# Optimization experiments

Measured on AMD Instinct MI355X. Metric: run time of the kernel, lower is better.

Reference implementation:

```python
import jax, jax.numpy as jnp
import numpy as np

NV, NE, H, P = 50000, 10000, 256, 400000

def setup_inputs() -> dict:
    key = jax.random.key(0)
    ks = jax.random.split(key, 16)
    s = 1.0 / np.sqrt(H)
    return {
        "v": jax.random.normal(ks[0], (NV, H), jnp.float32),
        "e": jax.random.normal(ks[1], (NE, H), jnp.float32),
        "W_v2e_w": jax.random.normal(ks[2], (H, H), jnp.float32) * s,
        "W_v2e_b": jnp.zeros((H,), jnp.float32),
        "W_e2v_w": jax.random.normal(ks[3], (H, H), jnp.float32) * s,
        "W_e2v_b": jnp.zeros((H,), jnp.float32),
        "n_weight": jax.random.uniform(ks[4], (NV, 1), jnp.float32),
        "e_weight": jax.random.uniform(ks[5], (NE, 1), jnp.float32),
        "n_reg_weight": jax.random.uniform(ks[6], (P, 1), jnp.float32),
        "e_reg_weight": jax.random.uniform(ks[7], (P, 1), jnp.float32),
        "e_reg_sum": jax.random.uniform(ks[8], (NE, 1), jnp.float32) + 1.0,  # positive normalizer
        "n_reg_sum": jax.random.uniform(ks[9], (NV, 1), jnp.float32) + 1.0,
        "pairs_v": jax.random.randint(ks[10], (P,), 0, NV, jnp.int32),  # ve_lists[:,0]
        "eidx": jax.random.randint(ks[11], (P,), 0, NE, jnp.int32),
        "pairs_e": jax.random.randint(ks[12], (P,), 0, NE, jnp.int32),  # ve_lists[:,1]
        "vidx": jax.random.randint(ks[13], (P,), 0, NV, jnp.int32),
    }

def reference(v, e, W_v2e_w, W_v2e_b, W_e2v_w, W_e2v_b, n_weight, e_weight,
              n_reg_weight, e_reg_weight, e_reg_sum, n_reg_sum,
              pairs_v, eidx, pairs_e, vidx):
    # v2e: dense transform on vertices, gather per incidence, scatter-add into edges
    ve = jax.nn.relu(v @ W_v2e_w.T + W_v2e_b)            # [NV,H]
    v_acc = v * n_weight                                 # v *= n_weight * v_fac(=1)
    msg_ve = (ve * n_weight)[pairs_v] * n_reg_weight     # [P,H]
    e_out = e.at[eidx].add(msg_ve) / e_reg_sum           # [NE,H]
    # e2v: dense transform on edges, gather per incidence, scatter-add into vertices
    ev = jax.nn.relu(e_out @ W_e2v_w.T + W_e2v_b)        # [NE,H]
    msg_ev = (ev * e_weight)[pairs_e] * e_reg_weight     # [P,H]
    v_out = v_acc.at[vidx].add(msg_ev) / n_reg_sum       # [NV,H]
    return v_out, e_out
```

## Files before the change

kernel.cpp:

```cpp
#include <hip/hip_runtime.h>
#include <stdint.h>

#define NV 50000
#define NE 10000
#define HD 256
#define NP 400000

#define SE 88
#define SV 36

#define NCH 128
#define CHP (NP / NCH)
#define NW  15000
#define NWE 2500
#define NWV 12500

#define PREP_HBLK NCH
#define PREP_WBLK 16

typedef short short8 __attribute__((ext_vector_type(8)));
typedef short short4v __attribute__((ext_vector_type(4)));
typedef float f32x4 __attribute__((ext_vector_type(4)));

__device__ __forceinline__ short f2bf(float f) {
    unsigned int u = __builtin_bit_cast(unsigned int, f);
    u += 0x7FFFu + ((u >> 16) & 1u);
    return (short)(u >> 16);
}
__device__ __forceinline__ float bf2f(short s) {
    unsigned int u = ((unsigned int)(unsigned short)s) << 16;
    return __builtin_bit_cast(float, u);
}

__global__ __launch_bounds__(1024) void prep_kernel(
    const float* __restrict__ W1, const float* __restrict__ W2,
    const int* __restrict__ eidx, const int* __restrict__ vidx,
    short* __restrict__ W_bf,
    int* __restrict__ cnt8)
{
    __shared__ int h[NW];
    int b = blockIdx.x;
    int tid = threadIdx.x;
    if (b < PREP_HBLK) {
        for (int w = tid; w < NW; w += 1024) h[w] = 0;
        __syncthreads();
        int base = b * CHP;
        for (int k = tid; k < CHP; k += 1024) {
            int p = base + k;
            int er = eidx[p];
            atomicAdd((unsigned*)&h[er >> 2], 1u << ((er & 3) * 8));
            int rv = 10000 + vidx[p];
            atomicAdd((unsigned*)&h[rv >> 2], 1u << ((rv & 3) * 8));
        }
        __syncthreads();
        for (int w = tid; w < NW; w += 1024) cnt8[b * NW + w] = h[w];
    } else {
        size_t i = (size_t)(b - PREP_HBLK) * 8192 + (size_t)tid * 8;
        const float* src = (i < 65536) ? (W1 + i) : (W2 + (i - 65536));
        float4 a0 = *(const float4*)src;
        float4 a1 = *(const float4*)(src + 4);
        short8 s;
        s[0] = f2bf(a0.x); s[1] = f2bf(a0.y); s[2] = f2bf(a0.z); s[3] = f2bf(a0.w);
        s[4] = f2bf(a1.x); s[5] = f2bf(a1.y); s[6] = f2bf(a1.z); s[7] = f2bf(a1.w);
        *(short8*)(W_bf + i) = s;
    }
}

__global__ __launch_bounds__(256) void scan_kernel(
    int* __restrict__ cnt8, int* __restrict__ cnt_e, int* __restrict__ cnt_v)
{
    int w = blockIdx.x * 256 + threadIdx.x;
    if (w >= NW) return;
    unsigned acc = 0;
#pragma unroll 8
    for (int c = 0; c < NCH; ++c) {
        unsigned x = (unsigned)cnt8[c * NW + w];
        cnt8[c * NW + w] = (int)acc;
        acc += x;
    }
    int r0 = w * 4;
    int4 t;
    t.x = acc & 0xFF; t.y = (acc >> 8) & 0xFF; t.z = (acc >> 16) & 0xFF; t.w = acc >> 24;
    if (r0 < 10000) *(int4*)&cnt_e[r0] = t;
    else            *(int4*)&cnt_v[r0 - 10000] = t;
}

__global__ __launch_bounds__(1024) void place_kernel(
    const int* __restrict__ eidx, const int* __restrict__ vidx,
    const int* __restrict__ pairs_v, const int* __restrict__ n_reg_w_bits,
    const int* __restrict__ pairs_e, const int* __restrict__ e_reg_w_bits,
    const int* __restrict__ cnt8,
    int2* __restrict__ bkt_e, int2* __restrict__ bkt_v)
{
    __shared__ int h[NWV];
    int b = blockIdx.x;
    int tid = threadIdx.x;
    if (b < NCH) {
        int c = b;
        for (int w = tid; w < NWE; w += 1024) h[w] = cnt8[c * NW + w];
        __syncthreads();
        int base = c * CHP;
        for (int k = tid; k < CHP; k += 1024) {
            int p = base + k;
            int er = eidx[p];
            unsigned old = atomicAdd((unsigned*)&h[er >> 2], 1u << ((er & 3) * 8));
            int s = (old >> ((er & 3) * 8)) & 0xFF;
            if (s < SE) bkt_e[er * SE + s] = make_int2(pairs_v[p], n_reg_w_bits[p]);
        }
    } else {
        int c = b - NCH;
        for (int w = tid; w < NWV; w += 1024) h[w] = cnt8[c * NW + NWE + w];
        __syncthreads();
        int base = c * CHP;
        for (int k = tid; k < CHP; k += 1024) {
            int p = base + k;
            int vr = vidx[p];
            unsigned old = atomicAdd((unsigned*)&h[vr >> 2], 1u << ((vr & 3) * 8));
            int s = (old >> ((vr & 3) * 8)) & 0xFF;
            if (s < SV) bkt_v[vr * SV + s] = make_int2(pairs_e[p], e_reg_w_bits[p]);
        }
    }
}

__global__ __launch_bounds__(256) void gemm_rs(
    const void* __restrict__ Av, int a_bf,
    const short* __restrict__ Wb,
    const float* __restrict__ bias,
    const float* __restrict__ rowscale,
    short* __restrict__ out,
    short* __restrict__ a_out,
    int M)
{
    __shared__ short As[64 * 256];
    __shared__ short Ws[64 * 256];
    const int tid  = threadIdx.x;
    const int row0 = blockIdx.x * 64;

#pragma unroll
    for (int it = 0; it < 8; ++it) {
        int cl = it * 256 + tid;
        int r  = cl >> 5;
        int c  = cl & 31;
        int gr0 = row0 + r;
        int gr  = gr0 < M ? gr0 : M - 1;
        short8 ap;
        if (a_bf) {
            ap = *(const short8*)((const short*)Av + (size_t)gr * HD + (c << 3));
        } else {
            const float* asrc = (const float*)Av + (size_t)gr * HD + (c << 3);
            float4 a0 = *(const float4*)asrc;
            float4 a1 = *(const float4*)(asrc + 4);
            ap[0] = f2bf(a0.x); ap[1] = f2bf(a0.y); ap[2] = f2bf(a0.z); ap[3] = f2bf(a0.w);
            ap[4] = f2bf(a1.x); ap[5] = f2bf(a1.y); ap[6] = f2bf(a1.z); ap[7] = f2bf(a1.w);
            if (a_out && gr0 < M)
                *(short8*)(a_out + (size_t)gr0 * HD + (c << 3)) = ap;
        }
        *(short8*)&As[(r << 8) + ((c ^ (r & 7)) << 3)] = ap;
    }

    const int lane = tid & 63;
    const int wv   = tid >> 6;
    const int m16  = lane & 15;
    const int quad = lane >> 4;
    const int arow = (wv << 4) + m16;

    for (int ct = 0; ct < 4; ++ct) {
        __syncthreads();
#pragma unroll
        for (int it = 0; it < 8; ++it) {
            int cl = it * 256 + tid;
            int r  = cl >> 5;
            int c  = cl & 31;
            short8 wp = *(const short8*)(Wb + (size_t)((ct << 6) + r) * HD + (c << 3));
            *(short8*)&Ws[(r << 8) + ((c ^ (r & 7)) << 3)] = wp;
        }
        __syncthreads();

        f32x4 acc[4];
#pragma unroll
        for (int nt = 0; nt < 4; ++nt) acc[nt] = (f32x4){0.f, 0.f, 0.f, 0.f};

#pragma unroll
        for (int ks = 0; ks < 8; ++ks) {
            int c = (ks << 2) + quad;
            short8 afr = *(const short8*)&As[(arow << 8) + ((c ^ (arow & 7)) << 3)];
#pragma unroll
            for (int nt = 0; nt < 4; ++nt) {
                int brow = (nt << 4) + m16;
                short8 bfr = *(const short8*)&Ws[(brow << 8) + ((c ^ (m16 & 7)) << 3)];
                acc[nt] = __builtin_amdgcn_mfma_f32_16x16x32_bf16(afr, bfr, acc[nt], 0, 0, 0);
            }
        }

#pragma unroll
        for (int r = 0; r < 4; ++r) {
            int row = row0 + (wv << 4) + (quad << 2) + r;
            if (row < M) {
                float rs = rowscale[row];
#pragma unroll
                for (int nt = 0; nt < 4; ++nt) {
                    int col = (ct << 6) + (nt << 4) + m16;
                    float val = acc[nt][r] + bias[col];
                    val = fmaxf(val, 0.0f) * rs;
                    out[(size_t)row * HD + col] = f2bf(val);
                }
            }
        }
    }
}

__device__ __forceinline__ void gather_win(
    const short* __restrict__ msg, int src, int wb, int cnt, int lane,
    float4& A, float4& B)
{
    int j = 0;
    for (; j + 8 <= cnt; j += 8) {
        int s0 = __shfl(src, j),     s1 = __shfl(src, j + 1);
        int s2 = __shfl(src, j + 2), s3 = __shfl(src, j + 3);
        int s4 = __shfl(src, j + 4), s5 = __shfl(src, j + 5);
        int s6 = __shfl(src, j + 6), s7 = __shfl(src, j + 7);
        float w0 = __builtin_bit_cast(float, __shfl(wb, j));
        float w1 = __builtin_bit_cast(float, __shfl(wb, j + 1));
        float w2 = __builtin_bit_cast(float, __shfl(wb, j + 2));
        float w3 = __builtin_bit_cast(float, __shfl(wb, j + 3));
        float w4 = __builtin_bit_cast(float, __shfl(wb, j + 4));
        float w5 = __builtin_bit_cast(float, __shfl(wb, j + 5));
        float w6 = __builtin_bit_cast(float, __shfl(wb, j + 6));
        float w7 = __builtin_bit_cast(float, __shfl(wb, j + 7));
        short4v m0 = *(const short4v*)(msg + ((size_t)s0 << 8) + (lane << 2));
        short4v m1 = *(const short4v*)(msg + ((size_t)s1 << 8) + (lane << 2));
        short4v m2 = *(const short4v*)(msg + ((size_t)s2 << 8) + (lane << 2));
        short4v m3 = *(const short4v*)(msg + ((size_t)s3 << 8) + (lane << 2));
        short4v m4 = *(const short4v*)(msg + ((size_t)s4 << 8) + (lane << 2));
        short4v m5 = *(const short4v*)(msg + ((size_t)s5 << 8) + (lane << 2));
        short4v m6 = *(const short4v*)(msg + ((size_t)s6 << 8) + (lane << 2));
        short4v m7 = *(const short4v*)(msg + ((size_t)s7 << 8) + (lane << 2));
        A.x += bf2f(m0[0]) * w0; A.y += bf2f(m0[1]) * w0;
        A.z += bf2f(m0[2]) * w0; A.w += bf2f(m0[3]) * w0;
        B.x += bf2f(m1[0]) * w1; B.y += bf2f(m1[1]) * w1;
        B.z += bf2f(m1[2]) * w1; B.w += bf2f(m1[3]) * w1;
        A.x += bf2f(m2[0]) * w2; A.y += bf2f(m2[1]) * w2;
        A.z += bf2f(m2[2]) * w2; A.w += bf2f(m2[3]) * w2;
        B.x += bf2f(m3[0]) * w3; B.y += bf2f(m3[1]) * w3;
        B.z += bf2f(m3[2]) * w3; B.w += bf2f(m3[3]) * w3;
        A.x += bf2f(m4[0]) * w4; A.y += bf2f(m4[1]) * w4;
        A.z += bf2f(m4[2]) * w4; A.w += bf2f(m4[3]) * w4;
        B.x += bf2f(m5[0]) * w5; B.y += bf2f(m5[1]) * w5;
        B.z += bf2f(m5[2]) * w5; B.w += bf2f(m5[3]) * w5;
        A.x += bf2f(m6[0]) * w6; A.y += bf2f(m6[1]) * w6;
        A.z += bf2f(m6[2]) * w6; A.w += bf2f(m6[3]) * w6;
        B.x += bf2f(m7[0]) * w7; B.y += bf2f(m7[1]) * w7;
        B.z += bf2f(m7[2]) * w7; B.w += bf2f(m7[3]) * w7;
    }
    for (; j + 2 <= cnt; j += 2) {
        int s0 = __shfl(src, j), s1 = __shfl(src, j + 1);
        float w0 = __builtin_bit_cast(float, __shfl(wb, j));
        float w1 = __builtin_bit_cast(float, __shfl(wb, j + 1));
        short4v m0 = *(const short4v*)(msg + ((size_t)s0 << 8) + (lane << 2));
        short4v m1 = *(const short4v*)(msg + ((size_t)s1 << 8) + (lane << 2));
        A.x += bf2f(m0[0]) * w0; A.y += bf2f(m0[1]) * w0;
        A.z += bf2f(m0[2]) * w0; A.w += bf2f(m0[3]) * w0;
        B.x += bf2f(m1[0]) * w1; B.y += bf2f(m1[1]) * w1;
        B.z += bf2f(m1[2]) * w1; B.w += bf2f(m1[3]) * w1;
    }
    if (j < cnt) {
        int s0 = __shfl(src, j);
        float w0 = __builtin_bit_cast(float, __shfl(wb, j));
        short4v m0 = *(const short4v*)(msg + ((size_t)s0 << 8) + (lane << 2));
        A.x += bf2f(m0[0]) * w0; A.y += bf2f(m0[1]) * w0;
        A.z += bf2f(m0[2]) * w0; A.w += bf2f(m0[3]) * w0;
    }
}

__global__ __launch_bounds__(256) void gather_e(
    const short* __restrict__ msg,
    const int2* __restrict__ bkt,
    const int* __restrict__ cnt,
    const float* __restrict__ e_in, const float* __restrict__ reg_sum,
    float* __restrict__ out, short* __restrict__ out_bf)
{
    int r    = (blockIdx.x << 2) + (threadIdx.x >> 6);
    int lane = threadIdx.x & 63;
    int i0 = r * SE;
    int2 q = bkt[i0 + lane];
    int n = cnt[r]; n = n < SE ? n : SE;
    float4 A = ((const float4*)(e_in + (size_t)r * HD))[lane];
    float4 B = {0.f, 0.f, 0.f, 0.f};
    float inv = 1.0f / reg_sum[r];
    int n0 = n < 64 ? n : 64;
    gather_win(msg, q.x, q.y, n0, lane, A, B);
    if (n > 64) {
        int2 q2 = make_int2(0, 0);
        if (lane < SE - 64) q2 = bkt[i0 + 64 + lane];
        gather_win(msg, q2.x, q2.y, n - 64, lane, A, B);
    }
    float4 acc;
    acc.x = (A.x + B.x) * inv; acc.y = (A.y + B.y) * inv;
    acc.z = (A.z + B.z) * inv; acc.w = (A.w + B.w) * inv;
    ((float4*)(out + (size_t)r * HD))[lane] = acc;
    if (out_bf) {
        short4v s;
        s[0] = f2bf(acc.x); s[1] = f2bf(acc.y); s[2] = f2bf(acc.z); s[3] = f2bf(acc.w);
        *(short4v*)(out_bf + (size_t)r * HD + (lane << 2)) = s;
    }
}

__global__ __launch_bounds__(256) void gather_v(
    const short* __restrict__ msg,
    const int2* __restrict__ bkt,
    const int* __restrict__ cnt,
    const float* __restrict__ v_f32, const short* __restrict__ v_bf,
    const float* __restrict__ n_w,
    const float* __restrict__ reg_sum, float* __restrict__ out)
{
    int r    = (blockIdx.x << 2) + (threadIdx.x >> 6);
    int lane = threadIdx.x & 63;
    int i0 = r * SV;
    int2 q = bkt[i0 + lane];
    int n = cnt[r]; n = n < SV ? n : SV;
    float nw = n_w[r];
    float inv = 1.0f / reg_sum[r];
    float4 a;
    if (v_bf) {
        short4v b = *(const short4v*)(v_bf + (size_t)r * HD + (lane << 2));
        a.x = bf2f(b[0]); a.y = bf2f(b[1]); a.z = bf2f(b[2]); a.w = bf2f(b[3]);
    } else {
        a = ((const float4*)(v_f32 + (size_t)r * HD))[lane];
    }
    float4 A; A.x = a.x * nw; A.y = a.y * nw; A.z = a.z * nw; A.w = a.w * nw;
    float4 B = {0.f, 0.f, 0.f, 0.f};
    gather_win(msg, q.x, q.y, n, lane, A, B);
    float4 acc;
    acc.x = (A.x + B.x) * inv; acc.y = (A.y + B.y) * inv;
    acc.z = (A.z + B.z) * inv; acc.w = (A.w + B.w) * inv;
    ((float4*)(out + (size_t)r * HD))[lane] = acc;
}

extern "C" void kernel_launch(void* const* d_in, const int* in_sizes, int n_in,
                              void* d_out, int out_size, void* d_ws, size_t ws_size,
                              hipStream_t stream) {
    const float* v   = (const float*)d_in[0];
    const float* e   = (const float*)d_in[1];
    const float* W1  = (const float*)d_in[2];
    const float* b1  = (const float*)d_in[3];
    const float* W2  = (const float*)d_in[4];
    const float* b2  = (const float*)d_in[5];
    const float* n_weight     = (const float*)d_in[6];
    const float* e_weight     = (const float*)d_in[7];
    const float* n_reg_weight = (const float*)d_in[8];
    const float* e_reg_weight = (const float*)d_in[9];
    const float* e_reg_sum    = (const float*)d_in[10];
    const float* n_reg_sum    = (const float*)d_in[11];
    const int* pairs_v = (const int*)d_in[12];
    const int* eidx    = (const int*)d_in[13];
    const int* pairs_e = (const int*)d_in[14];
    const int* vidx    = (const int*)d_in[15];

    float* out      = (float*)d_out;
    float* v_region = out;
    float* e_region = out + (size_t)NV * HD;

    char* ws = (char*)d_ws;
    size_t o = 0;
    short* msg     = (short*)(ws + o); o += (size_t)NV * HD * 2;
    int2*  bkt_e   = (int2*)(ws + o);  o += ((size_t)NE * SE + 64) * 8;
    int2*  bkt_v   = (int2*)(ws + o);  o += ((size_t)NV * SV + 64) * 8;
    short* W_bf    = (short*)(ws + o); o += (size_t)2 * 65536 * 2;
    int*   cnt8    = (int*)(ws + o);
    short* e_bf    = (short*)(ws + o); o += (size_t)NCH * NW * 4;
    int*   cnt_e   = (int*)(ws + o);   o += (size_t)NE * 4;
    int*   cnt_v   = (int*)(ws + o);   o += (size_t)NV * 4;
    size_t o_opt = o;
    short* v_bf    = (short*)(ws + o_opt);
    size_t need_full = o_opt + (size_t)NV * HD * 2;
    const int full = (ws_size >= need_full);

    prep_kernel<<<PREP_HBLK + PREP_WBLK, 1024, 0, stream>>>(
        W1, W2, eidx, vidx, W_bf, cnt8);
    scan_kernel<<<(NW + 255) / 256, 256, 0, stream>>>(cnt8, cnt_e, cnt_v);
    place_kernel<<<2 * NCH, 1024, 0, stream>>>(
        eidx, vidx, pairs_v, (const int*)n_reg_weight,
        pairs_e, (const int*)e_reg_weight, cnt8, bkt_e, bkt_v);

    gemm_rs<<<(NV + 63) / 64, 256, 0, stream>>>(
        (const void*)v, 0, W_bf, b1, n_weight, msg, full ? v_bf : (short*)0, NV);
    gather_e<<<NE / 4, 256, 0, stream>>>(msg, bkt_e, cnt_e,
        e, e_reg_sum, e_region, e_bf);
    gemm_rs<<<(NE + 63) / 64, 256, 0, stream>>>(
        (const void*)e_bf, 1, W_bf + 65536, b2, e_weight, msg, (short*)0, NE);
    gather_v<<<NV / 4, 256, 0, stream>>>(msg, bkt_v, cnt_v,
        v, full ? v_bf : (short*)0, n_weight, n_reg_sum, v_region);
}
```

Before: 282.5 us.

## Load GEMM operands directly into registers and drop bf16 copy of v

Measured after the change: 322.7 us. 1.14x slower.

```diff
diff --git a/kernel.cpp b/kernel.cpp
--- a/kernel.cpp
+++ b/kernel.cpp
@@ -128,67 +128,49 @@
     const float* __restrict__ bias,
     const float* __restrict__ rowscale,
     short* __restrict__ out,
-    short* __restrict__ a_out,
     int M)
 {
-    __shared__ short As[64 * 256];
-    __shared__ short Ws[64 * 256];
     const int tid  = threadIdx.x;
-    const int row0 = blockIdx.x * 64;
-
-#pragma unroll
-    for (int it = 0; it < 8; ++it) {
-        int cl = it * 256 + tid;
-        int r  = cl >> 5;
-        int c  = cl & 31;
-        int gr0 = row0 + r;
-        int gr  = gr0 < M ? gr0 : M - 1;
-        short8 ap;
-        if (a_bf) {
-            ap = *(const short8*)((const short*)Av + (size_t)gr * HD + (c << 3));
-        } else {
-            const float* asrc = (const float*)Av + (size_t)gr * HD + (c << 3);
-            float4 a0 = *(const float4*)asrc;
-            float4 a1 = *(const float4*)(asrc + 4);
-            ap[0] = f2bf(a0.x); ap[1] = f2bf(a0.y); ap[2] = f2bf(a0.z); ap[3] = f2bf(a0.w);
-            ap[4] = f2bf(a1.x); ap[5] = f2bf(a1.y); ap[6] = f2bf(a1.z); ap[7] = f2bf(a1.w);
-            if (a_out && gr0 < M)
-                *(short8*)(a_out + (size_t)gr0 * HD + (c << 3)) = ap;
-        }
-        *(short8*)&As[(r << 8) + ((c ^ (r & 7)) << 3)] = ap;
-    }
-
     const int lane = tid & 63;
     const int wv   = tid >> 6;
     const int m16  = lane & 15;
     const int quad = lane >> 4;
     const int arow = (wv << 4) + m16;
+    const int row0 = blockIdx.x * 64;
+    int gr0 = row0 + arow;
+    int gr  = gr0 < M ? gr0 : M - 1;
+
+    short8 a_frag[8];
+    if (a_bf) {
+        const short* asrc = (const short*)Av + (size_t)gr * HD + (quad << 3);
+#pragma unroll
+        for (int ks = 0; ks < 8; ++ks)
+            a_frag[ks] = *(const short8*)(asrc + (ks << 5));
+    } else {
+        const float* asrc = (const float*)Av + (size_t)gr * HD + (quad << 3);
+#pragma unroll
+        for (int ks = 0; ks < 8; ++ks) {
+            float4 a0 = *(const float4*)(asrc + (ks << 5));
+            float4 a1 = *(const float4*)(asrc + (ks << 5) + 4);
+            short8 ap;
+            ap[0] = f2bf(a0.x); ap[1] = f2bf(a0.y); ap[2] = f2bf(a0.z); ap[3] = f2bf(a0.w);
+            ap[4] = f2bf(a1.x); ap[5] = f2bf(a1.y); ap[6] = f2bf(a1.z); ap[7] = f2bf(a1.w);
+            a_frag[ks] = ap;
+        }
+    }
 
     for (int ct = 0; ct < 4; ++ct) {
-        __syncthreads();
-#pragma unroll
-        for (int it = 0; it < 8; ++it) {
-            int cl = it * 256 + tid;
-            int r  = cl >> 5;
-            int c  = cl & 31;
-            short8 wp = *(const short8*)(Wb + (size_t)((ct << 6) + r) * HD + (c << 3));
-            *(short8*)&Ws[(r << 8) + ((c ^ (r & 7)) << 3)] = wp;
-        }
-        __syncthreads();
-
         f32x4 acc[4];
 #pragma unroll
         for (int nt = 0; nt < 4; ++nt) acc[nt] = (f32x4){0.f, 0.f, 0.f, 0.f};
 
+        const short* wbase = Wb + (size_t)((ct << 6) + m16) * HD + (quad << 3);
 #pragma unroll
         for (int ks = 0; ks < 8; ++ks) {
-            int c = (ks << 2) + quad;
-            short8 afr = *(const short8*)&As[(arow << 8) + ((c ^ (arow & 7)) << 3)];
 #pragma unroll
             for (int nt = 0; nt < 4; ++nt) {
-                int brow = (nt << 4) + m16;
-                short8 bfr = *(const short8*)&Ws[(brow << 8) + ((c ^ (m16 & 7)) << 3)];
-                acc[nt] = __builtin_amdgcn_mfma_f32_16x16x32_bf16(afr, bfr, acc[nt], 0, 0, 0);
+                short8 bfr = *(const short8*)(wbase + ((size_t)(nt << 4) * HD) + (ks << 5));
+                acc[nt] = __builtin_amdgcn_mfma_f32_16x16x32_bf16(a_frag[ks], bfr, acc[nt], 0, 0, 0);
             }
         }
 
@@ -309,7 +291,7 @@
     const short* __restrict__ msg,
     const int2* __restrict__ bkt,
     const int* __restrict__ cnt,
-    const float* __restrict__ v_f32, const short* __restrict__ v_bf,
+    const float* __restrict__ v_f32,
     const float* __restrict__ n_w,
     const float* __restrict__ reg_sum, float* __restrict__ out)
 {
@@ -320,13 +302,7 @@
     int n = cnt[r]; n = n < SV ? n : SV;
     float nw = n_w[r];
     float inv = 1.0f / reg_sum[r];
-    float4 a;
-    if (v_bf) {
-        short4v b = *(const short4v*)(v_bf + (size_t)r * HD + (lane << 2));
-        a.x = bf2f(b[0]); a.y = bf2f(b[1]); a.z = bf2f(b[2]); a.w = bf2f(b[3]);
-    } else {
-        a = ((const float4*)(v_f32 + (size_t)r * HD))[lane];
-    }
+    float4 a = ((const float4*)(v_f32 + (size_t)r * HD))[lane];
     float4 A; A.x = a.x * nw; A.y = a.y * nw; A.z = a.z * nw; A.w = a.w * nw;
     float4 B = {0.f, 0.f, 0.f, 0.f};
     gather_win(msg, q.x, q.y, n, lane, A, B);
@@ -370,10 +346,6 @@
     short* e_bf    = (short*)(ws + o); o += (size_t)NCH * NW * 4;
     int*   cnt_e   = (int*)(ws + o);   o += (size_t)NE * 4;
     int*   cnt_v   = (int*)(ws + o);   o += (size_t)NV * 4;
-    size_t o_opt = o;
-    short* v_bf    = (short*)(ws + o_opt);
-    size_t need_full = o_opt + (size_t)NV * HD * 2;
-    const int full = (ws_size >= need_full);
 
     prep_kernel<<<PREP_HBLK + PREP_WBLK, 1024, 0, stream>>>(
         W1, W2, eidx, vidx, W_bf, cnt8);
@@ -383,11 +355,11 @@
         pairs_e, (const int*)e_reg_weight, cnt8, bkt_e, bkt_v);
 
     gemm_rs<<<(NV + 63) / 64, 256, 0, stream>>>(
-        (const void*)v, 0, W_bf, b1, n_weight, msg, full ? v_bf : (short*)0, NV);
+        (const void*)v, 0, W_bf, b1, n_weight, msg, NV);
     gather_e<<<NE / 4, 256, 0, stream>>>(msg, bkt_e, cnt_e,
         e, e_reg_sum, e_region, e_bf);
     gemm_rs<<<(NE + 63) / 64, 256, 0, stream>>>(
-        (const void*)e_bf, 1, W_bf + 65536, b2, e_weight, msg, (short*)0, NE);
+        (const void*)e_bf, 1, W_bf + 65536, b2, e_weight, msg, NE);
     gather_v<<<NV / 4, 256, 0, stream>>>(msg, bkt_v, cnt_v,
-        v, full ? v_bf : (short*)0, n_weight, n_reg_sum, v_region);
-}
+        v, n_weight, n_reg_sum, v_region);
+}
```
